# Optimization experiments

Hardware: AMD Instinct MI355X
Metric: run time of the kernel (lower is better)

The kernel has to match this reference:

```python
import jax, jax.numpy as jnp
import numpy as np

H = 1024
HEADS = 16
FFN = 2048
EPS = 1e-5


def _layernorm(x, g, b):
    mu = jnp.mean(x, axis=-1, keepdims=True)
    var = jnp.mean(jnp.square(x - mu), axis=-1, keepdims=True)
    return (x - mu) * jax.lax.rsqrt(var + EPS) * g + b


def setup_inputs() -> dict:
    key = jax.random.key(0)
    ks = jax.random.split(key, 8)
    N, L = 4, 1024
    s = 1.0 / np.sqrt(H)
    inp = {
        "src_hidden": jax.random.normal(ks[0], (N, L, H), dtype=jnp.float32),
        "src_mask": jnp.ones((N, L), dtype=jnp.int32),
        "Wq": jax.random.normal(ks[1], (H, H), dtype=jnp.float32) * s,
        "bq": jnp.zeros((H,), jnp.float32),
        "Wk": jax.random.normal(ks[2], (H, H), dtype=jnp.float32) * s,
        "bk": jnp.zeros((H,), jnp.float32),
        "Wv": jax.random.normal(ks[3], (H, H), dtype=jnp.float32) * s,
        "bv": jnp.zeros((H,), jnp.float32),
        "Wo": jax.random.normal(ks[4], (H, H), dtype=jnp.float32) * s,
        "bo": jnp.zeros((H,), jnp.float32),
        "ln1_g": jnp.ones((H,), jnp.float32),
        "ln1_b": jnp.zeros((H,), jnp.float32),
        "W1": jax.random.normal(ks[5], (H, FFN), dtype=jnp.float32) * s,
        "b1": jnp.zeros((FFN,), jnp.float32),
        "W2": jax.random.normal(ks[6], (FFN, H), dtype=jnp.float32) * (1.0 / np.sqrt(FFN)),
        "b2": jnp.zeros((H,), jnp.float32),
        "ln2_g": jnp.ones((H,), jnp.float32),
        "ln2_b": jnp.zeros((H,), jnp.float32),
    }
    return inp


def reference(src_hidden, src_mask, Wq, bq, Wk, bk, Wv, bv, Wo, bo,
              ln1_g, ln1_b, W1, b1, W2, b2, ln2_g, ln2_b):
    N, L, _ = src_hidden.shape
    d = H // HEADS
    scale = 1.0 / np.sqrt(H)  # applied to BOTH Q and K, as in the original
    # NOTE: head split is a plain reshape (view), faithful to the original code
    Q = ((src_hidden @ Wq + bq).reshape(N, HEADS, L, d)) * scale
    K = ((src_hidden @ Wk + bk).reshape(N, HEADS, L, d)) * scale
    V = (src_hidden @ Wv + bv).reshape(N, HEADS, L, d)
    sims = jnp.einsum('nhid,nhjd->nhij', Q, K)  # (N, heads, L, L)
    mask = src_mask[:, None, None, :]  # (N,1,1,L) broadcasts over heads and query dim
    sims = jnp.where(mask == 0, -jnp.inf, sims)
    attn = jax.nn.softmax(sims, axis=-1)
    ctx = jnp.einsum('nhij,nhjd->nhid', attn, V)
    concats = ctx.reshape(N, L, H)
    hid = concats @ Wo + bo
    x1 = _layernorm(hid, ln1_g, ln1_b) + hid
    ffn = jax.nn.relu(x1 @ W1 + b1) @ W2 + b2  # dropout is identity in eval
    out = _layernorm(ffn, ln2_g, ln2_b) + ffn
    return (out, src_mask)
```

## Files before the change

kernel.cpp:

```cpp
#include <hip/hip_runtime.h>
#include <math.h>

#define H 1024
#define HEADS 16
#define DH 64
#define FFN_DIM 2048
#define EPS 1e-5f
#define NB 4
#define LL 1024
#define M_ROWS 4096

typedef __attribute__((ext_vector_type(8))) short bf16x8;
typedef __attribute__((ext_vector_type(4))) float f32x4;

__device__ __forceinline__ ushort f2bf(float x) {
    union { float f; unsigned u; } c; c.f = x;
    unsigned u = c.u;
    u += 0x7FFFu + ((u >> 16) & 1u);
    return (ushort)(u >> 16);
}

#define GLL(gp, lp)                                                         \
    __builtin_amdgcn_global_load_lds(                                       \
        (const __attribute__((address_space(1))) void*)(gp),                \
        (__attribute__((address_space(3))) void*)(lp), 16, 0, 0)

#define WAITV8() asm volatile("s_waitcnt vmcnt(8)" ::: "memory")
#define WAITV4() asm volatile("s_waitcnt vmcnt(4)" ::: "memory")
#define WAITV0() asm volatile("s_waitcnt vmcnt(0)" ::: "memory")
#define BAR() __builtin_amdgcn_s_barrier()

__global__ __launch_bounds__(256)
void gemm_bf16(const ushort* __restrict__ A, const ushort* __restrict__ Bt,
               const float* __restrict__ bias, float* __restrict__ Cf,
               ushort* __restrict__ Cb, int M, int N, int K,
               int relu, int qkv)
{
    __shared__ ushort As[3][128 * 32];
    __shared__ ushort Bs[3][128 * 32];
    const int tid = threadIdx.x;
    const int l = tid & 63, w = tid >> 6;
    const int wr = w >> 1, wc = w & 1;
    const int brow = blockIdx.y * 128, bcol = blockIdx.x * 128;
    const int NS = K >> 5;

    const ushort* Abase = A + (size_t)brow * K;
    const ushort* Bbase = Bt + (size_t)bcol * K;

    f32x4 acc[4][4];
    #pragma unroll
    for (int mi = 0; mi < 4; ++mi)
        #pragma unroll
        for (int ni = 0; ni < 4; ++ni)
            acc[mi][ni] = (f32x4)0.0f;

    auto stage = [&](int buf, int k0) {
        #pragma unroll
        for (int i = 0; i < 2; ++i) {
            const int f = i * 256 + tid;
            const int row = f >> 2, cp = f & 3;
            const int c = cp ^ ((row >> 1) & 3);
            const ushort* ga = Abase + (size_t)row * K + k0 + c * 8;
            const ushort* gb = Bbase + (size_t)row * K + k0 + c * 8;
            ushort* la = As[buf] + (size_t)(i * 256 + w * 64) * 8;
            ushort* lb = Bs[buf] + (size_t)(i * 256 + w * 64) * 8;
            GLL(ga, la);
            GLL(gb, lb);
        }
    };

    stage(0, 0);
    stage(1, 32);
    int scur = 0;
    for (int t = 0; t < NS; ++t) {
        int snext = scur + 2; if (snext >= 3) snext -= 3;
        if (t + 2 < NS) stage(snext, (t + 2) << 5);
        if (t < NS - 2)       WAITV8();
        else if (t == NS - 2) WAITV4();
        else                  WAITV0();
        BAR();

        bf16x8 af[4], bf[4];
        #pragma unroll
        for (int mi = 0; mi < 4; ++mi) {
            const int row = wr * 64 + mi * 16 + (l & 15);
            const int cc = (l >> 4) ^ ((row >> 1) & 3);
            af[mi] = *(const bf16x8*)&As[scur][row * 32 + cc * 8];
        }
        #pragma unroll
        for (int ni = 0; ni < 4; ++ni) {
            const int row = wc * 64 + ni * 16 + (l & 15);
            const int cc = (l >> 4) ^ ((row >> 1) & 3);
            bf[ni] = *(const bf16x8*)&Bs[scur][row * 32 + cc * 8];
        }
        __builtin_amdgcn_s_setprio(1);
        #pragma unroll
        for (int mi = 0; mi < 4; ++mi)
            #pragma unroll
            for (int ni = 0; ni < 4; ++ni)
                acc[mi][ni] = __builtin_amdgcn_mfma_f32_16x16x32_bf16(
                    af[mi], bf[ni], acc[mi][ni], 0, 0, 0);
        __builtin_amdgcn_s_setprio(0);
        BAR();
        scur = scur + 1 == 3 ? 0 : scur + 1;
    }

    const int colg0 = bcol + wc * 64 + (l & 15);
    const int rbase = brow + wr * 64 + ((l >> 4) << 2);
    const int seg   = qkv ? (bcol >> 10) : 0;
    const int Nw    = qkv ? 1024 : N;
    ushort* outb    = qkv ? (Cb + (size_t)seg * 4194304u) : Cb;
    #pragma unroll
    for (int ni = 0; ni < 4; ++ni) {
        const int colg = colg0 + ni * 16;
        const int colw = qkv ? (colg & 1023) : colg;
        const float bv = bias[colg];
        #pragma unroll
        for (int mi = 0; mi < 4; ++mi) {
            #pragma unroll
            for (int j = 0; j < 4; ++j) {
                float v = acc[mi][ni][j] + bv;
                if (relu) v = fmaxf(v, 0.0f);
                const size_t off = (size_t)(rbase + mi * 16 + j) * Nw + colw;
                if (Cf) Cf[off] = v;
                if (Cb) outb[off] = f2bf(v);
            }
        }
    }
}

__global__ __launch_bounds__(256)
void transpose_qkvo(const float* __restrict__ Wq, const float* __restrict__ Wk,
                    const float* __restrict__ Wv, const float* __restrict__ Wo,
                    ushort* __restrict__ Dq, ushort* __restrict__ Dk,
                    ushort* __restrict__ Dv, ushort* __restrict__ Do_)
{
    const float* W; ushort* D; float sc;
    switch (blockIdx.z) {
        case 0:  W = Wq; D = Dq;  sc = 0.03125f; break;
        case 1:  W = Wk; D = Dk;  sc = 0.03125f; break;
        case 2:  W = Wv; D = Dv;  sc = 1.0f;     break;
        default: W = Wo; D = Do_; sc = 1.0f;     break;
    }
    __shared__ float t[32][33];
    const int n0 = blockIdx.x * 32, k0 = blockIdx.y * 32;
    const int tx = threadIdx.x & 31, ty = threadIdx.x >> 5;
    #pragma unroll
    for (int r = 0; r < 4; ++r)
        t[ty + r * 8][tx] = W[(size_t)(k0 + ty + r * 8) * H + n0 + tx];
    __syncthreads();
    #pragma unroll
    for (int r = 0; r < 4; ++r)
        D[(size_t)(n0 + ty + r * 8) * H + k0 + tx] =
            f2bf(t[tx][ty + r * 8] * sc);
}

__global__ __launch_bounds__(256)
void transpose_to_bf16(const float* __restrict__ W, ushort* __restrict__ Wt,
                       int K, int N, float scale)
{
    __shared__ float t[32][33];
    const int n0 = blockIdx.x * 32, k0 = blockIdx.y * 32;
    const int tx = threadIdx.x & 31, ty = threadIdx.x >> 5;
    #pragma unroll
    for (int r = 0; r < 4; ++r)
        t[ty + r * 8][tx] = W[(size_t)(k0 + ty + r * 8) * N + n0 + tx];
    __syncthreads();
    #pragma unroll
    for (int r = 0; r < 4; ++r)
        Wt[(size_t)(n0 + ty + r * 8) * K + k0 + tx] =
            f2bf(t[tx][ty + r * 8] * scale);
}

__global__ __launch_bounds__(256)
void transpose_v(const ushort* __restrict__ V, ushort* __restrict__ Vt)
{
    const int nh = blockIdx.y, jt = blockIdx.x;
    const size_t base = (size_t)nh << 16;
    __shared__ ushort t[64][68];
    const int tid = threadIdx.x;
    #pragma unroll
    for (int pass = 0; pass < 4; ++pass) {
        const int j = pass * 16 + (tid >> 4);
        const int d0 = (tid & 15) * 4;
        ushort4 v = *(const ushort4*)&V[base + (size_t)(jt * 64 + j) * 64 + d0];
        t[d0 + 0][j] = v.x; t[d0 + 1][j] = v.y;
        t[d0 + 2][j] = v.z; t[d0 + 3][j] = v.w;
    }
    __syncthreads();
    #pragma unroll
    for (int pass = 0; pass < 4; ++pass) {
        const int d = pass * 16 + (tid >> 4);
        const int j0 = (tid & 15) * 4;
        ushort4 o;
        o.x = t[d][j0 + 0]; o.y = t[d][j0 + 1];
        o.z = t[d][j0 + 2]; o.w = t[d][j0 + 3];
        *(ushort4*)&Vt[base + (size_t)d * 1024 + jt * 64 + j0] = o;
    }
}

__global__ __launch_bounds__(256)
void f32_to_bf16(const float* __restrict__ in, ushort* __restrict__ out, int n4)
{
    const int i = blockIdx.x * blockDim.x + threadIdx.x;
    if (i < n4) {
        float4 v = *reinterpret_cast<const float4*>(&in[i * 4]);
        ushort4 o;
        o.x = f2bf(v.x); o.y = f2bf(v.y); o.z = f2bf(v.z); o.w = f2bf(v.w);
        *reinterpret_cast<ushort4*>(&out[i * 4]) = o;
    }
}

__global__ void build_bias_qkv(const float* __restrict__ bq,
                               const float* __restrict__ bk,
                               const float* __restrict__ bv,
                               float* __restrict__ out)
{
    const int i = blockIdx.x * 256 + threadIdx.x;
    if (i >= 3072) return;
    float v;
    if (i < 1024) v = bq[i] * 0.03125f;
    else if (i < 2048) v = bk[i - 1024] * 0.03125f;
    else v = bv[i - 2048];
    out[i] = v;
}

__global__ void mask_flags(const int* __restrict__ mask, int* __restrict__ fl)
{
    const int t = threadIdx.x;
    if (t < NB * 16) {
        const int n = t >> 4, tile = t & 15;
        int any = 0;
        for (int j = 0; j < 64; ++j)
            any |= (mask[n * LL + tile * 64 + j] == 0);
        fl[t] = any;
    }
}

__global__ __launch_bounds__(256)
void attn_mfma(const ushort* __restrict__ Q, const ushort* __restrict__ K,
               const ushort* __restrict__ Vt, const int* __restrict__ mask,
               const int* __restrict__ mflags, ushort* __restrict__ ctx)
{
    const int nh = blockIdx.y;
    const int n  = nh >> 4;
    const int qb = blockIdx.x;
    const size_t hb = (size_t)nh << 16;
    const ushort* Qh = Q + hb;
    const ushort* Kh = K + hb;
    const ushort* Vh = Vt + hb;
    ushort* Ch = ctx + hb;

    __shared__ ushort Ks[2][64 * 64];
    __shared__ ushort Vs[2][64 * 64];
    __shared__ ushort Ps[4][16 * 64];

    const int tid = threadIdx.x;
    const int l = tid & 63, w = tid >> 6;
    const int g = l >> 4, c0 = l & 15;

    unsigned fbits = 0;
    #pragma unroll
    for (int tt = 0; tt < 16; ++tt)
        fbits |= (unsigned)(mflags[n * 16 + tt] != 0) << tt;

    const ushort* qrow = Qh + (size_t)(qb * 64 + w * 16 + c0) * 64;
    const bf16x8 qf0 = *(const bf16x8*)(qrow + g * 8);
    const bf16x8 qf1 = *(const bf16x8*)(qrow + 32 + g * 8);

    f32x4 Oacc[4];
    #pragma unroll
    for (int nd = 0; nd < 4; ++nd) Oacc[nd] = (f32x4)0.0f;
    float lp[4] = {0.0f, 0.0f, 0.0f, 0.0f};

    auto stage = [&](int buf, int t) {
        #pragma unroll
        for (int i = 0; i < 2; ++i) {
            const int slot = i * 256 + tid;
            const int r = slot >> 3, p = slot & 7;
            const int c = p ^ (r & 7);
            const ushort* gk = Kh + (size_t)(t * 64 + r) * 64 + c * 8;
            const ushort* gv = Vh + (size_t)r * 1024 + t * 64 + c * 8;
            ushort* lk = Ks[buf] + (size_t)(i * 256 + w * 64) * 8;
            ushort* lv = Vs[buf] + (size_t)(i * 256 + w * 64) * 8;
            GLL(gk, lk);
            GLL(gv, lv);
        }
    };

    stage(0, 0);
    int cur = 0;
    for (int t = 0; t < 16; ++t) {
        if (t < 15) { stage(cur ^ 1, t + 1); WAITV4(); }
        else        { WAITV0(); }
        BAR();

        f32x4 s[4];
        #pragma unroll
        for (int nb = 0; nb < 4; ++nb) {
            s[nb] = (f32x4)0.0f;
            const int row = nb * 16 + c0;
            const int cc0 = g ^ (row & 7);
            const int cc1 = (4 + g) ^ (row & 7);
            bf16x8 kf0 = *(const bf16x8*)&Ks[cur][row * 64 + cc0 * 8];
            bf16x8 kf1 = *(const bf16x8*)&Ks[cur][row * 64 + cc1 * 8];
            __builtin_amdgcn_s_setprio(1);
            s[nb] = __builtin_amdgcn_mfma_f32_16x16x32_bf16(qf0, kf0, s[nb], 0, 0, 0);
            s[nb] = __builtin_amdgcn_mfma_f32_16x16x32_bf16(qf1, kf1, s[nb], 0, 0, 0);
            __builtin_amdgcn_s_setprio(0);
        }
        if (fbits >> t & 1) {
            #pragma unroll
            for (int nb = 0; nb < 4; ++nb) {
                const float mb =
                    mask[n * LL + t * 64 + nb * 16 + c0] ? 0.0f : -INFINITY;
                #pragma unroll
                for (int jr = 0; jr < 4; ++jr) s[nb][jr] += mb;
            }
        }
        #pragma unroll
        for (int nb = 0; nb < 4; ++nb)
            #pragma unroll
            for (int jr = 0; jr < 4; ++jr) {
                const float pv = __expf(s[nb][jr]);
                s[nb][jr] = pv;
                lp[jr] += pv;
            }

        ushort* Pw = Ps[w];
        #pragma unroll
        for (int nb = 0; nb < 4; ++nb) {
            const int chunkL = nb * 2 + (c0 >> 3);
            #pragma unroll
            for (int jr = 0; jr < 4; ++jr) {
                const int row = g * 4 + jr;
                const int pch = chunkL ^ (row & 7);
                Pw[row * 64 + pch * 8 + (c0 & 7)] = f2bf(s[nb][jr]);
            }
        }
        const bf16x8 pa0 = *(const bf16x8*)&Pw[c0 * 64 + ((g) ^ (c0 & 7)) * 8];
        const bf16x8 pa1 = *(const bf16x8*)&Pw[c0 * 64 + ((4 + g) ^ (c0 & 7)) * 8];
        #pragma unroll
        for (int nd = 0; nd < 4; ++nd) {
            const int row = nd * 16 + c0;
            const int cc0 = g ^ (row & 7);
            const int cc1 = (4 + g) ^ (row & 7);
            bf16x8 vf0 = *(const bf16x8*)&Vs[cur][row * 64 + cc0 * 8];
            bf16x8 vf1 = *(const bf16x8*)&Vs[cur][row * 64 + cc1 * 8];
            __builtin_amdgcn_s_setprio(1);
            Oacc[nd] = __builtin_amdgcn_mfma_f32_16x16x32_bf16(pa0, vf0, Oacc[nd], 0, 0, 0);
            Oacc[nd] = __builtin_amdgcn_mfma_f32_16x16x32_bf16(pa1, vf1, Oacc[nd], 0, 0, 0);
            __builtin_amdgcn_s_setprio(0);
        }
        BAR();
        cur ^= 1;
    }

    float inv[4];
    #pragma unroll
    for (int jr = 0; jr < 4; ++jr) {
        float v = lp[jr];
        #pragma unroll
        for (int off = 1; off < 16; off <<= 1) v += __shfl_xor(v, off, 64);
        inv[jr] = 1.0f / v;
    }
    #pragma unroll
    for (int nd = 0; nd < 4; ++nd) {
        #pragma unroll
        for (int jr = 0; jr < 4; ++jr) {
            const int row = qb * 64 + w * 16 + g * 4 + jr;
            Ch[(size_t)row * 64 + nd * 16 + c0] = f2bf(Oacc[nd][jr] * inv[jr]);
        }
    }
}

__global__ __launch_bounds__(256)
void ln_residual(const float* __restrict__ X, const float* __restrict__ g,
                 const float* __restrict__ b, float* __restrict__ outf,
                 ushort* __restrict__ outb)
{
    const int row = blockIdx.x;
    const int tid = threadIdx.x;
    const float* x = X + (size_t)row * H;
    float4 xv = *reinterpret_cast<const float4*>(&x[tid * 4]);
    float s = xv.x + xv.y + xv.z + xv.w;
    __shared__ float red[8];
    const int lane = tid & 63, wave = tid >> 6;
    #pragma unroll
    for (int off = 32; off > 0; off >>= 1) s += __shfl_down(s, off);
    if (lane == 0) red[wave] = s;
    __syncthreads();
    if (tid == 0)
        red[0] = (red[0] + red[1] + red[2] + red[3]) * (1.0f / H);
    __syncthreads();
    const float mu = red[0];
    const float d0 = xv.x - mu, d1 = xv.y - mu, d2 = xv.z - mu, d3 = xv.w - mu;
    float s2 = d0 * d0 + d1 * d1 + d2 * d2 + d3 * d3;
    #pragma unroll
    for (int off = 32; off > 0; off >>= 1) s2 += __shfl_down(s2, off);
    if (lane == 0) red[4 + wave] = s2;
    __syncthreads();
    if (tid == 0) {
        const float var = (red[4] + red[5] + red[6] + red[7]) * (1.0f / H);
        red[4] = rsqrtf(var + EPS);
    }
    __syncthreads();
    const float rstd = red[4];
    float4 gv = *reinterpret_cast<const float4*>(&g[tid * 4]);
    float4 bv = *reinterpret_cast<const float4*>(&b[tid * 4]);
    float4 ov;
    ov.x = d0 * rstd * gv.x + bv.x + xv.x;
    ov.y = d1 * rstd * gv.y + bv.y + xv.y;
    ov.z = d2 * rstd * gv.z + bv.z + xv.z;
    ov.w = d3 * rstd * gv.w + bv.w + xv.w;
    if (outf)
        *reinterpret_cast<float4*>(&outf[(size_t)row * H + tid * 4]) = ov;
    if (outb) {
        ushort4 ob;
        ob.x = f2bf(ov.x); ob.y = f2bf(ov.y);
        ob.z = f2bf(ov.z); ob.w = f2bf(ov.w);
        *reinterpret_cast<ushort4*>(&outb[(size_t)row * H + tid * 4]) = ob;
    }
}

__global__ void mask_to_float(const int* __restrict__ m, float* __restrict__ o,
                              int n)
{
    const int i = blockIdx.x * blockDim.x + threadIdx.x;
    if (i < n) o[i] = (float)m[i];
}

extern "C" void kernel_launch(void* const* d_in, const int* in_sizes, int n_in,
                              void* d_out, int out_size, void* d_ws, size_t ws_size,
                              hipStream_t stream)
{
    const float* X    = (const float*)d_in[0];
    const int*   mask = (const int*)d_in[1];
    const float* Wq   = (const float*)d_in[2];
    const float* bq   = (const float*)d_in[3];
    const float* Wk   = (const float*)d_in[4];
    const float* bk   = (const float*)d_in[5];
    const float* Wv   = (const float*)d_in[6];
    const float* bv   = (const float*)d_in[7];
    const float* Wo   = (const float*)d_in[8];
    const float* bo   = (const float*)d_in[9];
    const float* g1   = (const float*)d_in[10];
    const float* bln1 = (const float*)d_in[11];
    const float* W1   = (const float*)d_in[12];
    const float* b1   = (const float*)d_in[13];
    const float* W2   = (const float*)d_in[14];
    const float* b2   = (const float*)d_in[15];
    const float* g2   = (const float*)d_in[16];
    const float* bln2 = (const float*)d_in[17];

    char* wsb = (char*)d_ws;
    const size_t MB = 1u << 20;
    ushort* Qb16 = (ushort*)(wsb);
    float*  hid  = (float*)(wsb);
    float*  ffn  = (float*)(wsb);
    ushort* x1b  = (ushort*)(wsb + 16 * MB);
    ushort* Vb16 = (ushort*)(wsb + 16 * MB);
    ushort* Xb   = (ushort*)(wsb + 24 * MB);
    ushort* Vtb  = (ushort*)(wsb + 24 * MB);
    ushort* ctxb = (ushort*)(wsb + 32 * MB);
    ushort* Wqkvt = (ushort*)(wsb + 40 * MB);
    ushort* Wot   = (ushort*)(wsb + 46 * MB);
    ushort* W1t   = (ushort*)(wsb + 40 * MB);
    ushort* W2t   = (ushort*)(wsb + 44 * MB);
    float*  biasqkv = (float*)(wsb + 48 * MB);
    int*    mfl     = (int*)(wsb + 48 * MB + 16384);
    ushort* Fb      = (ushort*)(wsb + 48 * MB);

    dim3 blk(256);

    f32_to_bf16<<<dim3(M_ROWS * H / 4 / 256), blk, 0, stream>>>(X, Xb, M_ROWS * H / 4);
    transpose_qkvo<<<dim3(32, 32, 4), blk, 0, stream>>>(
        Wq, Wk, Wv, Wo, Wqkvt, Wqkvt + 1024 * 1024, Wqkvt + 2048 * 1024, Wot);
    build_bias_qkv<<<dim3(12), blk, 0, stream>>>(bq, bk, bv, biasqkv);
    mask_flags<<<dim3(1), dim3(64), 0, stream>>>(mask, mfl);

    gemm_bf16<<<dim3(24, 32), blk, 0, stream>>>(Xb, Wqkvt, biasqkv, nullptr, Qb16,
                                                M_ROWS, 3072, H, 0, 1);
    transpose_v<<<dim3(16, NB * HEADS), blk, 0, stream>>>(Vb16, Vtb);

    attn_mfma<<<dim3(16, NB * HEADS), blk, 0, stream>>>(
        Qb16, Qb16 + 4194304u, Vtb, mask, mfl, ctxb);

    gemm_bf16<<<dim3(8, 32), blk, 0, stream>>>(ctxb, Wot, bo, hid, nullptr,
                                               M_ROWS, H, H, 0, 0);
    ln_residual<<<dim3(M_ROWS), blk, 0, stream>>>(hid, g1, bln1, nullptr, x1b);

    transpose_to_bf16<<<dim3(FFN_DIM / 32, H / 32), blk, 0, stream>>>(W1, W1t, H, FFN_DIM, 1.0f);
    transpose_to_bf16<<<dim3(H / 32, FFN_DIM / 32), blk, 0, stream>>>(W2, W2t, FFN_DIM, H, 1.0f);

    gemm_bf16<<<dim3(16, 32), blk, 0, stream>>>(x1b, W1t, b1, nullptr, Fb,
                                                M_ROWS, FFN_DIM, H, 1, 0);
    gemm_bf16<<<dim3(8, 32), blk, 0, stream>>>(Fb, W2t, b2, ffn, nullptr,
                                               M_ROWS, H, FFN_DIM, 0, 0);

    ln_residual<<<dim3(M_ROWS), blk, 0, stream>>>(ffn, g2, bln2, (float*)d_out, nullptr);

    mask_to_float<<<dim3((NB * LL + 255) / 256), blk, 0, stream>>>(
        mask, (float*)d_out + (size_t)M_ROWS * H, NB * LL);
}
```

Measured before the change: 216.4 us.

## Use 512-thread GEMM blocks and split-K for N=1024 GEMMs, reducing in LayerNorm

The GEMM kernel now runs 8 waves per block, each computing a 64x32 sub-tile, and each thread issues one async load per operand per stage. The two N=1024 GEMMs (output projection and FFN down-projection) split K across two z-slices that write separate fp32 partials. The following LayerNorm kernel sums the partials, and only the first slice adds the bias. The aim is more waves in flight and twice as many blocks for the smaller GEMMs, which otherwise launch only 256 blocks. The cost is an extra fp32 partial write and read plus a workspace buffer reshuffle.

Result: faster. 197.3 us (-8.8%).

```diff
diff --git a/kernel.cpp b/kernel.cpp
--- a/kernel.cpp
+++ b/kernel.cpp
@@ -25,48 +25,47 @@
         (const __attribute__((address_space(1))) void*)(gp),                \
         (__attribute__((address_space(3))) void*)(lp), 16, 0, 0)
 
-#define WAITV8() asm volatile("s_waitcnt vmcnt(8)" ::: "memory")
 #define WAITV4() asm volatile("s_waitcnt vmcnt(4)" ::: "memory")
+#define WAITV2() asm volatile("s_waitcnt vmcnt(2)" ::: "memory")
 #define WAITV0() asm volatile("s_waitcnt vmcnt(0)" ::: "memory")
 #define BAR() __builtin_amdgcn_s_barrier()
 
-__global__ __launch_bounds__(256)
+__global__ __launch_bounds__(512, 6)
 void gemm_bf16(const ushort* __restrict__ A, const ushort* __restrict__ Bt,
-               const float* __restrict__ bias, float* __restrict__ Cf,
-               ushort* __restrict__ Cb, int M, int N, int K,
-               int relu, int qkv)
+               const float* __restrict__ bias, float* __restrict__ Cf0,
+               float* __restrict__ Cf1, ushort* __restrict__ Cb,
+               int M, int N, int K, int relu, int qkv)
 {
     __shared__ ushort As[3][128 * 32];
     __shared__ ushort Bs[3][128 * 32];
     const int tid = threadIdx.x;
     const int l = tid & 63, w = tid >> 6;
-    const int wr = w >> 1, wc = w & 1;
+    const int wr = w >> 2, wc = w & 3;
+    const int g = l >> 4, c0 = l & 15;
     const int brow = blockIdx.y * 128, bcol = blockIdx.x * 128;
-    const int NS = K >> 5;
-
-    const ushort* Abase = A + (size_t)brow * K;
-    const ushort* Bbase = Bt + (size_t)bcol * K;
-
-    f32x4 acc[4][4];
+    const int z = blockIdx.z;
+    const int Ksub = K / gridDim.z;
+    const int NS = Ksub >> 5;
+
+    const ushort* Abase = A + (size_t)brow * K + (size_t)z * Ksub;
+    const ushort* Bbase = Bt + (size_t)bcol * K + (size_t)z * Ksub;
+
+    f32x4 acc[4][2];
     #pragma unroll
     for (int mi = 0; mi < 4; ++mi)
         #pragma unroll
-        for (int ni = 0; ni < 4; ++ni)
+        for (int ni = 0; ni < 2; ++ni)
             acc[mi][ni] = (f32x4)0.0f;
 
     auto stage = [&](int buf, int k0) {
-        #pragma unroll
-        for (int i = 0; i < 2; ++i) {
-            const int f = i * 256 + tid;
-            const int row = f >> 2, cp = f & 3;
-            const int c = cp ^ ((row >> 1) & 3);
-            const ushort* ga = Abase + (size_t)row * K + k0 + c * 8;
-            const ushort* gb = Bbase + (size_t)row * K + k0 + c * 8;
-            ushort* la = As[buf] + (size_t)(i * 256 + w * 64) * 8;
-            ushort* lb = Bs[buf] + (size_t)(i * 256 + w * 64) * 8;
-            GLL(ga, la);
-            GLL(gb, lb);
-        }
+        const int row = tid >> 2, cp = tid & 3;
+        const int c = cp ^ ((row >> 1) & 3);
+        const ushort* ga = Abase + (size_t)row * K + k0 + c * 8;
+        const ushort* gb = Bbase + (size_t)row * K + k0 + c * 8;
+        ushort* la = As[buf] + (size_t)w * 512;
+        ushort* lb = Bs[buf] + (size_t)w * 512;
+        GLL(ga, la);
+        GLL(gb, lb);
     };
 
     stage(0, 0);
@@ -75,29 +74,29 @@
     for (int t = 0; t < NS; ++t) {
         int snext = scur + 2; if (snext >= 3) snext -= 3;
         if (t + 2 < NS) stage(snext, (t + 2) << 5);
-        if (t < NS - 2)       WAITV8();
-        else if (t == NS - 2) WAITV4();
+        if (t < NS - 2)       WAITV4();
+        else if (t == NS - 2) WAITV2();
         else                  WAITV0();
         BAR();
 
-        bf16x8 af[4], bf[4];
+        bf16x8 af[4], bf[2];
         #pragma unroll
         for (int mi = 0; mi < 4; ++mi) {
-            const int row = wr * 64 + mi * 16 + (l & 15);
-            const int cc = (l >> 4) ^ ((row >> 1) & 3);
+            const int row = wr * 64 + mi * 16 + c0;
+            const int cc = g ^ ((row >> 1) & 3);
             af[mi] = *(const bf16x8*)&As[scur][row * 32 + cc * 8];
         }
         #pragma unroll
-        for (int ni = 0; ni < 4; ++ni) {
-            const int row = wc * 64 + ni * 16 + (l & 15);
-            const int cc = (l >> 4) ^ ((row >> 1) & 3);
+        for (int ni = 0; ni < 2; ++ni) {
+            const int row = wc * 32 + ni * 16 + c0;
+            const int cc = g ^ ((row >> 1) & 3);
             bf[ni] = *(const bf16x8*)&Bs[scur][row * 32 + cc * 8];
         }
         __builtin_amdgcn_s_setprio(1);
         #pragma unroll
         for (int mi = 0; mi < 4; ++mi)
             #pragma unroll
-            for (int ni = 0; ni < 4; ++ni)
+            for (int ni = 0; ni < 2; ++ni)
                 acc[mi][ni] = __builtin_amdgcn_mfma_f32_16x16x32_bf16(
                     af[mi], bf[ni], acc[mi][ni], 0, 0, 0);
         __builtin_amdgcn_s_setprio(0);
@@ -105,16 +104,17 @@
         scur = scur + 1 == 3 ? 0 : scur + 1;
     }
 
-    const int colg0 = bcol + wc * 64 + (l & 15);
-    const int rbase = brow + wr * 64 + ((l >> 4) << 2);
+    float* Cf = (z == 0) ? Cf0 : Cf1;
+    const int colg0 = bcol + wc * 32 + c0;
+    const int rbase = brow + wr * 64 + (g << 2);
     const int seg   = qkv ? (bcol >> 10) : 0;
     const int Nw    = qkv ? 1024 : N;
     ushort* outb    = qkv ? (Cb + (size_t)seg * 4194304u) : Cb;
     #pragma unroll
-    for (int ni = 0; ni < 4; ++ni) {
+    for (int ni = 0; ni < 2; ++ni) {
         const int colg = colg0 + ni * 16;
         const int colw = qkv ? (colg & 1023) : colg;
-        const float bv = bias[colg];
+        const float bv = (z == 0) ? bias[colg] : 0.0f;
         #pragma unroll
         for (int mi = 0; mi < 4; ++mi) {
             #pragma unroll
@@ -375,14 +375,17 @@
 }
 
 __global__ __launch_bounds__(256)
-void ln_residual(const float* __restrict__ X, const float* __restrict__ g,
-                 const float* __restrict__ b, float* __restrict__ outf,
-                 ushort* __restrict__ outb)
+void ln_residual(const float* __restrict__ X, const float* __restrict__ X2,
+                 const float* __restrict__ g, const float* __restrict__ b,
+                 float* __restrict__ outf, ushort* __restrict__ outb)
 {
     const int row = blockIdx.x;
     const int tid = threadIdx.x;
-    const float* x = X + (size_t)row * H;
-    float4 xv = *reinterpret_cast<const float4*>(&x[tid * 4]);
+    float4 xv = *reinterpret_cast<const float4*>(&X[(size_t)row * H + tid * 4]);
+    if (X2) {
+        float4 yv = *reinterpret_cast<const float4*>(&X2[(size_t)row * H + tid * 4]);
+        xv.x += yv.x; xv.y += yv.y; xv.z += yv.z; xv.w += yv.w;
+    }
     float s = xv.x + xv.y + xv.z + xv.w;
     __shared__ float red[8];
     const int lane = tid & 63, wave = tid >> 6;
@@ -456,22 +459,24 @@
     char* wsb = (char*)d_ws;
     const size_t MB = 1u << 20;
     ushort* Qb16 = (ushort*)(wsb);
-    float*  hid  = (float*)(wsb);
-    float*  ffn  = (float*)(wsb);
-    ushort* x1b  = (ushort*)(wsb + 16 * MB);
     ushort* Vb16 = (ushort*)(wsb + 16 * MB);
     ushort* Xb   = (ushort*)(wsb + 24 * MB);
-    ushort* Vtb  = (ushort*)(wsb + 24 * MB);
-    ushort* ctxb = (ushort*)(wsb + 32 * MB);
+    ushort* ctxb = (ushort*)(wsb + 24 * MB);
+    ushort* Vtb  = (ushort*)(wsb + 32 * MB);
     ushort* Wqkvt = (ushort*)(wsb + 40 * MB);
     ushort* Wot   = (ushort*)(wsb + 46 * MB);
     ushort* W1t   = (ushort*)(wsb + 40 * MB);
     ushort* W2t   = (ushort*)(wsb + 44 * MB);
     float*  biasqkv = (float*)(wsb + 48 * MB);
     int*    mfl     = (int*)(wsb + 48 * MB + 16384);
+    float*  P1      = (float*)(wsb + 48 * MB);
     ushort* Fb      = (ushort*)(wsb + 48 * MB);
-
-    dim3 blk(256);
+    float*  P0  = (float*)(wsb);
+    ushort* x1b = (ushort*)(wsb + 16 * MB);
+    float*  Q0  = (float*)(wsb);
+    float*  Q1  = (float*)(wsb + 24 * MB);
+
+    dim3 blk(256), gblk(512);
 
     f32_to_bf16<<<dim3(M_ROWS * H / 4 / 256), blk, 0, stream>>>(X, Xb, M_ROWS * H / 4);
     transpose_qkvo<<<dim3(32, 32, 4), blk, 0, stream>>>(
@@ -479,26 +484,26 @@
     build_bias_qkv<<<dim3(12), blk, 0, stream>>>(bq, bk, bv, biasqkv);
     mask_flags<<<dim3(1), dim3(64), 0, stream>>>(mask, mfl);
 
-    gemm_bf16<<<dim3(24, 32), blk, 0, stream>>>(Xb, Wqkvt, biasqkv, nullptr, Qb16,
-                                                M_ROWS, 3072, H, 0, 1);
+    gemm_bf16<<<dim3(24, 32, 1), gblk, 0, stream>>>(
+        Xb, Wqkvt, biasqkv, nullptr, nullptr, Qb16, M_ROWS, 3072, H, 0, 1);
     transpose_v<<<dim3(16, NB * HEADS), blk, 0, stream>>>(Vb16, Vtb);
 
     attn_mfma<<<dim3(16, NB * HEADS), blk, 0, stream>>>(
         Qb16, Qb16 + 4194304u, Vtb, mask, mfl, ctxb);
 
-    gemm_bf16<<<dim3(8, 32), blk, 0, stream>>>(ctxb, Wot, bo, hid, nullptr,
-                                               M_ROWS, H, H, 0, 0);
-    ln_residual<<<dim3(M_ROWS), blk, 0, stream>>>(hid, g1, bln1, nullptr, x1b);
+    gemm_bf16<<<dim3(8, 32, 2), gblk, 0, stream>>>(
+        ctxb, Wot, bo, P0, P1, nullptr, M_ROWS, H, H, 0, 0);
+    ln_residual<<<dim3(M_ROWS), blk, 0, stream>>>(P0, P1, g1, bln1, nullptr, x1b);
 
     transpose_to_bf16<<<dim3(FFN_DIM / 32, H / 32), blk, 0, stream>>>(W1, W1t, H, FFN_DIM, 1.0f);
     transpose_to_bf16<<<dim3(H / 32, FFN_DIM / 32), blk, 0, stream>>>(W2, W2t, FFN_DIM, H, 1.0f);
 
-    gemm_bf16<<<dim3(16, 32), blk, 0, stream>>>(x1b, W1t, b1, nullptr, Fb,
-                                                M_ROWS, FFN_DIM, H, 1, 0);
-    gemm_bf16<<<dim3(8, 32), blk, 0, stream>>>(Fb, W2t, b2, ffn, nullptr,
-                                               M_ROWS, H, FFN_DIM, 0, 0);
-
-    ln_residual<<<dim3(M_ROWS), blk, 0, stream>>>(ffn, g2, bln2, (float*)d_out, nullptr);
+    gemm_bf16<<<dim3(16, 32, 1), gblk, 0, stream>>>(
+        x1b, W1t, b1, nullptr, nullptr, Fb, M_ROWS, FFN_DIM, H, 1, 0);
+    gemm_bf16<<<dim3(8, 32, 2), gblk, 0, stream>>>(
+        Fb, W2t, b2, Q0, Q1, nullptr, M_ROWS, H, FFN_DIM, 0, 0);
+
+    ln_residual<<<dim3(M_ROWS), blk, 0, stream>>>(Q0, Q1, g2, bln2, (float*)d_out, nullptr);
 
     mask_to_float<<<dim3((NB * LL + 255) / 256), blk, 0, stream>>>(
         mask, (float*)d_out + (size_t)M_ROWS * H, NB * LL);
```
